# Performance work log

Hardware: AMD Instinct MI355X
Metric: run time of the kernel (lower is better)

Reference implementation:

```python
import jax, jax.numpy as jnp
import numpy as np

B, TGT, SRC, SRC_DIM, TGT_DIM = 4, 4096, 4096, 256, 256
NEG_BIG = 1.0e11   # additive mask constant from the torch code
CLAMP_MIN = -1.0e10


def setup_inputs() -> dict:
    key = jax.random.key(0)
    k1, k2, k3, k4 = jax.random.split(key, 4)
    h_t = jax.random.normal(k1, (B, TGT, TGT_DIM), dtype=jnp.float32)
    h_s = jax.random.normal(k2, (B, SRC, SRC_DIM), dtype=jnp.float32)
    m_s = jax.random.randint(k3, (B, SRC), 0, 2, dtype=jnp.int32)
    # linear_in: nn.Linear(src_dim, tgt_dim, bias=False) -> weight [tgt_dim, src_dim]
    lim = float(np.sqrt(1.0 / SRC_DIM))
    W_in = jax.random.uniform(k4, (TGT_DIM, SRC_DIM), dtype=jnp.float32, minval=-lim, maxval=lim)
    return {"h_t": h_t, "h_s": h_s, "m_s": m_s, "W_in": W_in}


def reference(h_t, h_s, m_s, W_in):
    # 'general' score: h_t @ (linear_in(h_s))^T
    energy = jnp.einsum("bsd,td->bst", h_s, W_in)          # (B, S, tgt_dim)
    scores = jnp.einsum("btd,bsd->bts", h_t, energy)        # (B, T, S)
    m = m_s.astype(scores.dtype)[:, None, :]                 # (B, 1, S)
    scores = scores * m - NEG_BIG * (1.0 - m)
    scores = jax.nn.softmax(jnp.maximum(scores, CLAMP_MIN), axis=-1)
    context = jnp.einsum("bts,bsd->btd", scores, h_s)        # (B, T, src_dim)
    return context, scores
```

## Files before the change

### kernel.cpp

```cpp
#include <hip/hip_runtime.h>
#include <cstdint>
#include <cstddef>

typedef _Float16 f16;
typedef _Float16 half8 __attribute__((ext_vector_type(8)));
typedef float floatx4 __attribute__((ext_vector_type(4)));
typedef unsigned short ushort8 __attribute__((ext_vector_type(8)));

__device__ __forceinline__ void gload_lds16(const void* g, void* l) {
    __builtin_amdgcn_global_load_lds(
        (const __attribute__((address_space(1))) void*)g,
        (__attribute__((address_space(3))) void*)l,
        16, 0, 0);
}

__device__ __forceinline__ unsigned short f32_to_bf16(float f) {
    unsigned u = __float_as_uint(f);
    return (unsigned short)((u + 0x7FFFu + ((u >> 16) & 1u)) >> 16);
}
__device__ __forceinline__ float bf16_to_f32(unsigned short h) {
    return __uint_as_float(((unsigned)h) << 16);
}

__global__ void k_cvt(const float* __restrict__ src, f16* __restrict__ dst, int n8) {
    int i = blockIdx.x * blockDim.x + threadIdx.x;
    if (i >= n8) return;
    const float4* s = (const float4*)src + 2 * (size_t)i;
    float4 a = s[0], b = s[1];
    half8 h;
    h[0] = (f16)a.x; h[1] = (f16)a.y; h[2] = (f16)a.z; h[3] = (f16)a.w;
    h[4] = (f16)b.x; h[5] = (f16)b.y; h[6] = (f16)b.z; h[7] = (f16)b.w;
    ((half8*)dst)[i] = h;
}

__global__ void k_hs(const float* __restrict__ hs, f16* __restrict__ hs16, f16* __restrict__ hsT) {
    int id = blockIdx.x;
    int dt = id & 3;
    int st = (id >> 2) & 63;
    int b  = id >> 8;
    __shared__ f16 tile[64][65];
    int t = threadIdx.x;
    int s0 = st * 64, d0 = dt * 64;
#pragma unroll
    for (int i = 0; i < 16; i++) {
        int e = t + i * 256;
        int r = e >> 6, c = e & 63;
        float v = hs[((size_t)(b * 4096 + s0 + r)) * 256 + d0 + c];
        f16 hv = (f16)v;
        hs16[((size_t)(b * 4096 + s0 + r)) * 256 + d0 + c] = hv;
        tile[r][c] = hv;
    }
    __syncthreads();
#pragma unroll
    for (int i = 0; i < 16; i++) {
        int e = t + i * 256;
        int r = e >> 6, c = e & 63;
        hsT[((size_t)(b * 256 + d0 + r)) * 4096 + s0 + c] = tile[c][r];
    }
}

__global__ __launch_bounds__(256, 2) void k_energy(
    const f16* __restrict__ A,
    const f16* __restrict__ Bt,
    f16* __restrict__ C)
{
    int id = blockIdx.x;
    int tn = id & 1, tm = (id >> 1) & 31, b = id >> 6;
    const f16* Ab = A + (size_t)b * 4096 * 256;

    __shared__ __align__(16) f16 As[128 * 64];
    __shared__ __align__(16) f16 Bs[128 * 64];

    int tid = threadIdx.x;
    int wave = tid >> 6, lane = tid & 63;
    int wr = wave >> 1, wc = wave & 1;
    int lm = lane & 15, lq = lane >> 4;

    floatx4 acc[4][4] = {};
    int r0 = tm * 128, c0 = tn * 128;

    for (int k0 = 0; k0 < 256; k0 += 64) {
#pragma unroll
        for (int i = 0; i < 4; i++) {
            int rbase = wave * 32 + i * 8;
            int row = rbase + (lane >> 3);
            gload_lds16(Ab + (size_t)(r0 + row) * 256 + k0 + (lane & 7) * 8, &As[rbase * 64]);
            gload_lds16(Bt + (size_t)(c0 + row) * 256 + k0 + (lane & 7) * 8, &Bs[rbase * 64]);
        }
        __syncthreads();
        half8 af[4][2], bf[4][2];
#pragma unroll
        for (int mi = 0; mi < 4; mi++)
#pragma unroll
            for (int kk = 0; kk < 2; kk++) {
                af[mi][kk] = *(const half8*)&As[(wr * 64 + mi * 16 + lm) * 64 + kk * 32 + lq * 8];
                bf[mi][kk] = *(const half8*)&Bs[(wc * 64 + mi * 16 + lm) * 64 + kk * 32 + lq * 8];
            }
#pragma unroll
        for (int kk = 0; kk < 2; kk++)
#pragma unroll
            for (int mi = 0; mi < 4; mi++)
#pragma unroll
                for (int ni = 0; ni < 4; ni++)
                    acc[mi][ni] = __builtin_amdgcn_mfma_f32_16x16x32_f16(af[mi][kk], bf[ni][kk], acc[mi][ni], 0, 0, 0);
        __syncthreads();
    }
#pragma unroll
    for (int mi = 0; mi < 4; mi++)
#pragma unroll
        for (int ni = 0; ni < 4; ni++)
#pragma unroll
            for (int r = 0; r < 4; r++) {
                int row = r0 + wr * 64 + mi * 16 + lq * 4 + r;
                int col = c0 + wc * 64 + ni * 16 + lm;
                C[(size_t)(b * 4096 + row) * 256 + col] = (f16)acc[mi][ni][r];
            }
}

__global__ __launch_bounds__(256, 2) void k_scores(
    const f16* __restrict__ A,
    const f16* __restrict__ Bt,
    const int* __restrict__ ms,
    unsigned short* __restrict__ E,
    float* __restrict__ rsum)
{
    int id = blockIdx.x;
    int tn = id & 31, tm = (id >> 5) & 31, b = id >> 10;
    const f16* Ab = A + (size_t)b * 4096 * 256;
    const f16* Bb = Bt + (size_t)b * 4096 * 256;

    __shared__ __align__(16) f16 As[128 * 64];
    __shared__ __align__(16) f16 Bs[128 * 64];

    int tid = threadIdx.x;
    int wave = tid >> 6, lane = tid & 63;
    int wr = wave >> 1, wc = wave & 1;
    int lm = lane & 15, lq = lane >> 4;

    floatx4 acc[4][4] = {};
    int r0 = tm * 128, c0 = tn * 128;

    for (int k0 = 0; k0 < 256; k0 += 64) {
#pragma unroll
        for (int i = 0; i < 4; i++) {
            int rbase = wave * 32 + i * 8;
            int row = rbase + (lane >> 3);
            gload_lds16(Ab + (size_t)(r0 + row) * 256 + k0 + (lane & 7) * 8, &As[rbase * 64]);
            gload_lds16(Bb + (size_t)(c0 + row) * 256 + k0 + (lane & 7) * 8, &Bs[rbase * 64]);
        }
        __syncthreads();
        half8 af[4][2], bf[4][2];
#pragma unroll
        for (int mi = 0; mi < 4; mi++)
#pragma unroll
            for (int kk = 0; kk < 2; kk++) {
                af[mi][kk] = *(const half8*)&As[(wr * 64 + mi * 16 + lm) * 64 + kk * 32 + lq * 8];
                bf[mi][kk] = *(const half8*)&Bs[(wc * 64 + mi * 16 + lm) * 64 + kk * 32 + lq * 8];
            }
#pragma unroll
        for (int kk = 0; kk < 2; kk++)
#pragma unroll
            for (int mi = 0; mi < 4; mi++)
#pragma unroll
                for (int ni = 0; ni < 4; ni++)
                    acc[mi][ni] = __builtin_amdgcn_mfma_f32_16x16x32_f16(af[mi][kk], bf[ni][kk], acc[mi][ni], 0, 0, 0);
        __syncthreads();
    }
    float rs[4][4] = {};
#pragma unroll
    for (int ni = 0; ni < 4; ni++) {
        int col = c0 + wc * 64 + ni * 16 + lm;
        int m = ms[b * 4096 + col];
#pragma unroll
        for (int mi = 0; mi < 4; mi++)
#pragma unroll
            for (int r = 0; r < 4; r++) {
                int row = r0 + wr * 64 + mi * 16 + lq * 4 + r;
                float e = m ? __expf(acc[mi][ni][r]) : 0.0f;
                E[(size_t)(b * 4096 + row) * 4096 + col] = f32_to_bf16(e);
                rs[mi][r] += e;
            }
    }
#pragma unroll
    for (int mi = 0; mi < 4; mi++)
#pragma unroll
        for (int r = 0; r < 4; r++) {
            float v = rs[mi][r];
#pragma unroll
            for (int off = 1; off < 16; off <<= 1)
                v += __shfl_xor(v, off, 16);
            if (lm == 0) {
                int row = r0 + wr * 64 + mi * 16 + lq * 4 + r;
                atomicAdd(&rsum[b * 4096 + row], v);
            }
        }
}

__global__ __launch_bounds__(256, 2) void k_ctx(
    const f16* __restrict__ BtT,
    const unsigned short* __restrict__ E,
    float* __restrict__ P,
    const float* __restrict__ rsum,
    f16* __restrict__ part)
{
    int id = blockIdx.x;
    int ks = id & 3, tt = (id >> 2) & 31, b = id >> 7;
    int tid = threadIdx.x;
    int wave = tid >> 6, lane = tid & 63;
    int lm = lane & 15, lq = lane >> 4;

    __shared__ __align__(16) f16 Bs[8 * 2048];

    int t0 = tt * 128;
    const f16* Bb = BtT + (size_t)b * 256 * 4096;

    float rinv[2];
    size_t rowbase[2];
#pragma unroll
    for (int mi = 0; mi < 2; mi++) {
        int row = t0 + wave * 32 + mi * 16 + lm;
        int gr = b * 4096 + row;
        rinv[mi] = 1.0f / rsum[gr];
        rowbase[mi] = (size_t)gr * 4096;
    }

    int g0 = wave * 2, g1 = wave * 2 + 1;
    int c0g = 2 * (g0 & 3), c1g = 2 * (g1 & 3);
    const f16* gp0 = Bb + (size_t)(lane ^ c0g) * 4096 + g0 * 8;
    const f16* gp1 = Bb + (size_t)(lane ^ c1g) * 4096 + g1 * 8;
    f16* lb0 = &Bs[g0 * 2048];
    f16* lb1 = &Bs[g1 * 2048];

    int rbk[2];
    rbk[0] = (0 * 4 + lq) * 2048 + (lm ^ (2 * lq)) * 8;
    rbk[1] = (1 * 4 + lq) * 2048 + (lm ^ (2 * lq)) * 8;

    floatx4 acc[2][16] = {};
    int sbeg = ks * 1024;

    for (int it = 0; it < 16; it++) {
        int s0 = sbeg + it * 64;
        ushort8 ev[2][2];
#pragma unroll
        for (int mi = 0; mi < 2; mi++)
#pragma unroll
            for (int kk = 0; kk < 2; kk++)
                ev[mi][kk] = *(const ushort8*)(E + rowbase[mi] + s0 + kk * 32 + lq * 8);
#pragma unroll
        for (int R = 0; R < 256; R += 64) {
            gload_lds16(gp0 + (size_t)R * 4096 + s0, lb0 + R * 8);
            gload_lds16(gp1 + (size_t)R * 4096 + s0, lb1 + R * 8);
        }
        half8 af[2][2];
#pragma unroll
        for (int mi = 0; mi < 2; mi++)
#pragma unroll
            for (int kk = 0; kk < 2; kk++) {
                half8 h;
#pragma unroll
                for (int j = 0; j < 8; j++) {
                    float f = bf16_to_f32(ev[mi][kk][j]) * rinv[mi];
                    h[j] = (f16)f;
                }
                af[mi][kk] = h;
            }
        __syncthreads();
#pragma unroll
        for (int mi = 0; mi < 2; mi++)
#pragma unroll
            for (int kk = 0; kk < 2; kk++) {
                float* p = P + rowbase[mi] + s0 + kk * 32 + lq * 8;
                half8 h = af[mi][kk];
                ((float4*)p)[0] = make_float4((float)h[0], (float)h[1], (float)h[2], (float)h[3]);
                ((float4*)p)[1] = make_float4((float)h[4], (float)h[5], (float)h[6], (float)h[7]);
            }
#pragma unroll
        for (int kk = 0; kk < 2; kk++)
#pragma unroll
            for (int ni = 0; ni < 16; ni++) {
                half8 bf = *(const half8*)&Bs[rbk[kk] + ni * 128];
#pragma unroll
                for (int mi = 0; mi < 2; mi++)
                    acc[mi][ni] = __builtin_amdgcn_mfma_f32_16x16x32_f16(af[mi][kk], bf, acc[mi][ni], 0, 0, 0);
            }
        __syncthreads();
    }

    f16* Pp = part + (size_t)ks * 4194304 + (size_t)b * 1048576;
#pragma unroll
    for (int mi = 0; mi < 2; mi++)
#pragma unroll
        for (int ni = 0; ni < 16; ni++)
#pragma unroll
            for (int r = 0; r < 4; r++) {
                int row = t0 + wave * 32 + mi * 16 + lq * 4 + r;
                int col = ni * 16 + lm;
                Pp[(size_t)row * 256 + col] = (f16)acc[mi][ni][r];
            }
}

__global__ void k_red(const f16* __restrict__ part, float* __restrict__ out) {
    size_t i = (size_t)blockIdx.x * 256 + threadIdx.x;
    const half8* p = (const half8*)part;
    half8 a = p[i];
    half8 b = p[i + 524288];
    half8 c = p[i + 1048576];
    half8 d = p[i + 1572864];
    float4 o0, o1;
    o0.x = (float)a[0] + (float)b[0] + (float)c[0] + (float)d[0];
    o0.y = (float)a[1] + (float)b[1] + (float)c[1] + (float)d[1];
    o0.z = (float)a[2] + (float)b[2] + (float)c[2] + (float)d[2];
    o0.w = (float)a[3] + (float)b[3] + (float)c[3] + (float)d[3];
    o1.x = (float)a[4] + (float)b[4] + (float)c[4] + (float)d[4];
    o1.y = (float)a[5] + (float)b[5] + (float)c[5] + (float)d[5];
    o1.z = (float)a[6] + (float)b[6] + (float)c[6] + (float)d[6];
    o1.w = (float)a[7] + (float)b[7] + (float)c[7] + (float)d[7];
    ((float4*)out)[2 * i] = o0;
    ((float4*)out)[2 * i + 1] = o1;
}

extern "C" void kernel_launch(void* const* d_in, const int* in_sizes, int n_in,
                              void* d_out, int out_size, void* d_ws, size_t ws_size,
                              hipStream_t stream) {
    const float* h_t = (const float*)d_in[0];
    const float* h_s = (const float*)d_in[1];
    const int*   m_s = (const int*)d_in[2];
    const float* W   = (const float*)d_in[3];

    float* out = (float*)d_out;
    char* ws = (char*)d_ws;
    f16* h_t16 = (f16*)(ws);
    f16* h_s16 = (f16*)(ws + 8388608);
    f16* h_sT  = (f16*)(ws + 16777216);
    f16* en16  = (f16*)(ws + 25165824);
    f16* W16   = (f16*)(ws + 33554432);
    float* rsum = (float*)(ws + 33685504);
    unsigned short* e16 = (unsigned short*)(ws + 33751040);
    f16* part = (f16*)(ws + 167968768);

    float* ctx = out;
    float* sc  = out + 4194304;

    hipMemsetAsync(rsum, 0, 16384 * sizeof(float), stream);
    k_cvt<<<2048, 256, 0, stream>>>(h_t, h_t16, 524288);
    k_cvt<<<32, 256, 0, stream>>>(W, W16, 8192);
    k_hs<<<1024, 256, 0, stream>>>(h_s, h_s16, h_sT);
    k_energy<<<256, 256, 0, stream>>>(h_s16, W16, en16);
    k_scores<<<4096, 256, 0, stream>>>(h_t16, en16, m_s, e16, rsum);
    k_ctx<<<512, 256, 0, stream>>>(h_sT, e16, sc, rsum, part);
    k_red<<<2048, 256, 0, stream>>>(part, ctx);
}
```

Baseline: 501.2 us.

## Double-buffer LDS tiles in energy, scores and context GEMM kernels

Adds a second LDS buffer to the energy and scores GEMMs and unrolls the four K-steps so the next tile's global-to-LDS load is issued before computing on the current tile. This roughly halves the barriers per step. The context kernel gets a ping-pong LDS buffer and register prefetch of the next E chunk, overlapping memory latency with the MFMA work. LDS use doubles (64KB per block in the GEMMs) and register pressure rises, which may lower occupancy under the launch bound of 2 blocks.

```diff
diff --git a/kernel.cpp b/kernel.cpp
--- a/kernel.cpp
+++ b/kernel.cpp
@@ -59,6 +59,33 @@
     }
 }
 
+#define GE_STAGE(AS, BS, K0) do { \
+    _Pragma("unroll") \
+    for (int i_ = 0; i_ < 4; i_++) { \
+        int rbase_ = wave * 32 + i_ * 8; \
+        int row_ = rbase_ + (lane >> 3); \
+        gload_lds16(Ab + (size_t)(r0 + row_) * 256 + (K0) + (lane & 7) * 8, &AS[rbase_ * 64]); \
+        gload_lds16(Bsrc + (size_t)(c0 + row_) * 256 + (K0) + (lane & 7) * 8, &BS[rbase_ * 64]); \
+    } } while (0)
+
+#define GE_COMPUTE(AS, BS) do { \
+    half8 af_[4][2], bf_[4][2]; \
+    _Pragma("unroll") \
+    for (int mi_ = 0; mi_ < 4; mi_++) \
+        _Pragma("unroll") \
+        for (int kk_ = 0; kk_ < 2; kk_++) { \
+            af_[mi_][kk_] = *(const half8*)&AS[(wr * 64 + mi_ * 16 + lm) * 64 + kk_ * 32 + lq * 8]; \
+            bf_[mi_][kk_] = *(const half8*)&BS[(wc * 64 + mi_ * 16 + lm) * 64 + kk_ * 32 + lq * 8]; \
+        } \
+    _Pragma("unroll") \
+    for (int kk_ = 0; kk_ < 2; kk_++) \
+        _Pragma("unroll") \
+        for (int mi_ = 0; mi_ < 4; mi_++) \
+            _Pragma("unroll") \
+            for (int ni_ = 0; ni_ < 4; ni_++) \
+                acc[mi_][ni_] = __builtin_amdgcn_mfma_f32_16x16x32_f16(af_[mi_][kk_], bf_[ni_][kk_], acc[mi_][ni_], 0, 0, 0); \
+    } while (0)
+
 __global__ __launch_bounds__(256, 2) void k_energy(
     const f16* __restrict__ A,
     const f16* __restrict__ Bt,
@@ -67,9 +94,12 @@
     int id = blockIdx.x;
     int tn = id & 1, tm = (id >> 1) & 31, b = id >> 6;
     const f16* Ab = A + (size_t)b * 4096 * 256;
-
-    __shared__ __align__(16) f16 As[128 * 64];
-    __shared__ __align__(16) f16 Bs[128 * 64];
+    const f16* Bsrc = Bt;
+
+    __shared__ __align__(16) f16 As0[128 * 64];
+    __shared__ __align__(16) f16 Bs0[128 * 64];
+    __shared__ __align__(16) f16 As1[128 * 64];
+    __shared__ __align__(16) f16 Bs1[128 * 64];
 
     int tid = threadIdx.x;
     int wave = tid >> 6, lane = tid & 63;
@@ -79,32 +109,19 @@
     floatx4 acc[4][4] = {};
     int r0 = tm * 128, c0 = tn * 128;
 
-    for (int k0 = 0; k0 < 256; k0 += 64) {
-#pragma unroll
-        for (int i = 0; i < 4; i++) {
-            int rbase = wave * 32 + i * 8;
-            int row = rbase + (lane >> 3);
-            gload_lds16(Ab + (size_t)(r0 + row) * 256 + k0 + (lane & 7) * 8, &As[rbase * 64]);
-            gload_lds16(Bt + (size_t)(c0 + row) * 256 + k0 + (lane & 7) * 8, &Bs[rbase * 64]);
-        }
-        __syncthreads();
-        half8 af[4][2], bf[4][2];
-#pragma unroll
-        for (int mi = 0; mi < 4; mi++)
-#pragma unroll
-            for (int kk = 0; kk < 2; kk++) {
-                af[mi][kk] = *(const half8*)&As[(wr * 64 + mi * 16 + lm) * 64 + kk * 32 + lq * 8];
-                bf[mi][kk] = *(const half8*)&Bs[(wc * 64 + mi * 16 + lm) * 64 + kk * 32 + lq * 8];
-            }
-#pragma unroll
-        for (int kk = 0; kk < 2; kk++)
-#pragma unroll
-            for (int mi = 0; mi < 4; mi++)
-#pragma unroll
-                for (int ni = 0; ni < 4; ni++)
-                    acc[mi][ni] = __builtin_amdgcn_mfma_f32_16x16x32_f16(af[mi][kk], bf[ni][kk], acc[mi][ni], 0, 0, 0);
-        __syncthreads();
-    }
+    GE_STAGE(As0, Bs0, 0);
+    __syncthreads();
+    GE_STAGE(As1, Bs1, 64);
+    GE_COMPUTE(As0, Bs0);
+    __syncthreads();
+    GE_STAGE(As0, Bs0, 128);
+    GE_COMPUTE(As1, Bs1);
+    __syncthreads();
+    GE_STAGE(As1, Bs1, 192);
+    GE_COMPUTE(As0, Bs0);
+    __syncthreads();
+    GE_COMPUTE(As1, Bs1);
+
 #pragma unroll
     for (int mi = 0; mi < 4; mi++)
 #pragma unroll
@@ -127,10 +144,12 @@
     int id = blockIdx.x;
     int tn = id & 31, tm = (id >> 5) & 31, b = id >> 10;
     const f16* Ab = A + (size_t)b * 4096 * 256;
-    const f16* Bb = Bt + (size_t)b * 4096 * 256;
-
-    __shared__ __align__(16) f16 As[128 * 64];
-    __shared__ __align__(16) f16 Bs[128 * 64];
+    const f16* Bsrc = Bt + (size_t)b * 4096 * 256;
+
+    __shared__ __align__(16) f16 As0[128 * 64];
+    __shared__ __align__(16) f16 Bs0[128 * 64];
+    __shared__ __align__(16) f16 As1[128 * 64];
+    __shared__ __align__(16) f16 Bs1[128 * 64];
 
     int tid = threadIdx.x;
     int wave = tid >> 6, lane = tid & 63;
@@ -140,32 +159,19 @@
     floatx4 acc[4][4] = {};
     int r0 = tm * 128, c0 = tn * 128;
 
-    for (int k0 = 0; k0 < 256; k0 += 64) {
-#pragma unroll
-        for (int i = 0; i < 4; i++) {
-            int rbase = wave * 32 + i * 8;
-            int row = rbase + (lane >> 3);
-            gload_lds16(Ab + (size_t)(r0 + row) * 256 + k0 + (lane & 7) * 8, &As[rbase * 64]);
-            gload_lds16(Bb + (size_t)(c0 + row) * 256 + k0 + (lane & 7) * 8, &Bs[rbase * 64]);
-        }
-        __syncthreads();
-        half8 af[4][2], bf[4][2];
-#pragma unroll
-        for (int mi = 0; mi < 4; mi++)
-#pragma unroll
-            for (int kk = 0; kk < 2; kk++) {
-                af[mi][kk] = *(const half8*)&As[(wr * 64 + mi * 16 + lm) * 64 + kk * 32 + lq * 8];
-                bf[mi][kk] = *(const half8*)&Bs[(wc * 64 + mi * 16 + lm) * 64 + kk * 32 + lq * 8];
-            }
-#pragma unroll
-        for (int kk = 0; kk < 2; kk++)
-#pragma unroll
-            for (int mi = 0; mi < 4; mi++)
-#pragma unroll
-                for (int ni = 0; ni < 4; ni++)
-                    acc[mi][ni] = __builtin_amdgcn_mfma_f32_16x16x32_f16(af[mi][kk], bf[ni][kk], acc[mi][ni], 0, 0, 0);
-        __syncthreads();
-    }
+    GE_STAGE(As0, Bs0, 0);
+    __syncthreads();
+    GE_STAGE(As1, Bs1, 64);
+    GE_COMPUTE(As0, Bs0);
+    __syncthreads();
+    GE_STAGE(As0, Bs0, 128);
+    GE_COMPUTE(As1, Bs1);
+    __syncthreads();
+    GE_STAGE(As1, Bs1, 192);
+    GE_COMPUTE(As0, Bs0);
+    __syncthreads();
+    GE_COMPUTE(As1, Bs1);
+
     float rs[4][4] = {};
 #pragma unroll
     for (int ni = 0; ni < 4; ni++) {
@@ -209,7 +215,8 @@
     int wave = tid >> 6, lane = tid & 63;
     int lm = lane & 15, lq = lane >> 4;
 
-    __shared__ __align__(16) f16 Bs[8 * 2048];
+    __shared__ __align__(16) f16 Bs0[8 * 2048];
+    __shared__ __align__(16) f16 Bs1[8 * 2048];
 
     int t0 = tt * 128;
     const f16* Bb = BtT + (size_t)b * 256 * 4096;
@@ -228,8 +235,7 @@
     int c0g = 2 * (g0 & 3), c1g = 2 * (g1 & 3);
     const f16* gp0 = Bb + (size_t)(lane ^ c0g) * 4096 + g0 * 8;
     const f16* gp1 = Bb + (size_t)(lane ^ c1g) * 4096 + g1 * 8;
-    f16* lb0 = &Bs[g0 * 2048];
-    f16* lb1 = &Bs[g1 * 2048];
+    int lds_off0 = g0 * 2048, lds_off1 = g1 * 2048;
 
     int rbk[2];
     rbk[0] = (0 * 4 + lq) * 2048 + (lm ^ (2 * lq)) * 8;
@@ -238,53 +244,78 @@
     floatx4 acc[2][16] = {};
     int sbeg = ks * 1024;
 
-    for (int it = 0; it < 16; it++) {
-        int s0 = sbeg + it * 64;
-        ushort8 ev[2][2];
-#pragma unroll
-        for (int mi = 0; mi < 2; mi++)
-#pragma unroll
-            for (int kk = 0; kk < 2; kk++)
-                ev[mi][kk] = *(const ushort8*)(E + rowbase[mi] + s0 + kk * 32 + lq * 8);
-#pragma unroll
-        for (int R = 0; R < 256; R += 64) {
-            gload_lds16(gp0 + (size_t)R * 4096 + s0, lb0 + R * 8);
-            gload_lds16(gp1 + (size_t)R * 4096 + s0, lb1 + R * 8);
-        }
-        half8 af[2][2];
-#pragma unroll
-        for (int mi = 0; mi < 2; mi++)
-#pragma unroll
-            for (int kk = 0; kk < 2; kk++) {
-                half8 h;
-#pragma unroll
-                for (int j = 0; j < 8; j++) {
-                    float f = bf16_to_f32(ev[mi][kk][j]) * rinv[mi];
-                    h[j] = (f16)f;
-                }
-                af[mi][kk] = h;
-            }
-        __syncthreads();
-#pragma unroll
-        for (int mi = 0; mi < 2; mi++)
-#pragma unroll
-            for (int kk = 0; kk < 2; kk++) {
-                float* p = P + rowbase[mi] + s0 + kk * 32 + lq * 8;
-                half8 h = af[mi][kk];
-                ((float4*)p)[0] = make_float4((float)h[0], (float)h[1], (float)h[2], (float)h[3]);
-                ((float4*)p)[1] = make_float4((float)h[4], (float)h[5], (float)h[6], (float)h[7]);
-            }
+    ushort8 ev[2][2];
+#pragma unroll
+    for (int mi = 0; mi < 2; mi++)
 #pragma unroll
         for (int kk = 0; kk < 2; kk++)
-#pragma unroll
-            for (int ni = 0; ni < 16; ni++) {
-                half8 bf = *(const half8*)&Bs[rbk[kk] + ni * 128];
-#pragma unroll
-                for (int mi = 0; mi < 2; mi++)
-                    acc[mi][ni] = __builtin_amdgcn_mfma_f32_16x16x32_f16(af[mi][kk], bf, acc[mi][ni], 0, 0, 0);
-            }
-        __syncthreads();
-    }
+            ev[mi][kk] = *(const ushort8*)(E + rowbase[mi] + sbeg + kk * 32 + lq * 8);
+#pragma unroll
+    for (int R = 0; R < 256; R += 64) {
+        gload_lds16(gp0 + (size_t)R * 4096 + sbeg, &Bs0[lds_off0 + R * 8]);
+        gload_lds16(gp1 + (size_t)R * 4096 + sbeg, &Bs0[lds_off1 + R * 8]);
+    }
+    __syncthreads();
+
+#define CTX_ITER(IT, BSR, BSW) do { \
+    ushort8 evn_[2][2]; \
+    if ((IT) < 15) { \
+        int s0n_ = sbeg + ((IT) + 1) * 64; \
+        _Pragma("unroll") \
+        for (int mi = 0; mi < 2; mi++) \
+            _Pragma("unroll") \
+            for (int kk = 0; kk < 2; kk++) \
+                evn_[mi][kk] = *(const ushort8*)(E + rowbase[mi] + s0n_ + kk * 32 + lq * 8); \
+        _Pragma("unroll") \
+        for (int R = 0; R < 256; R += 64) { \
+            gload_lds16(gp0 + (size_t)R * 4096 + s0n_, &BSW[lds_off0 + R * 8]); \
+            gload_lds16(gp1 + (size_t)R * 4096 + s0n_, &BSW[lds_off1 + R * 8]); \
+        } \
+    } \
+    int s0c_ = sbeg + (IT) * 64; \
+    half8 af_[2][2]; \
+    _Pragma("unroll") \
+    for (int mi = 0; mi < 2; mi++) \
+        _Pragma("unroll") \
+        for (int kk = 0; kk < 2; kk++) { \
+            half8 h_; \
+            _Pragma("unroll") \
+            for (int j = 0; j < 8; j++) \
+                h_[j] = (f16)(bf16_to_f32(ev[mi][kk][j]) * rinv[mi]); \
+            af_[mi][kk] = h_; \
+        } \
+    _Pragma("unroll") \
+    for (int mi = 0; mi < 2; mi++) \
+        _Pragma("unroll") \
+        for (int kk = 0; kk < 2; kk++) { \
+            float* p_ = P + rowbase[mi] + s0c_ + kk * 32 + lq * 8; \
+            half8 h_ = af_[mi][kk]; \
+            ((float4*)p_)[0] = make_float4((float)h_[0], (float)h_[1], (float)h_[2], (float)h_[3]); \
+            ((float4*)p_)[1] = make_float4((float)h_[4], (float)h_[5], (float)h_[6], (float)h_[7]); \
+        } \
+    _Pragma("unroll") \
+    for (int kk = 0; kk < 2; kk++) \
+        _Pragma("unroll") \
+        for (int ni = 0; ni < 16; ni++) { \
+            half8 bf_ = *(const half8*)&BSR[rbk[kk] + ni * 128]; \
+            _Pragma("unroll") \
+            for (int mi = 0; mi < 2; mi++) \
+                acc[mi][ni] = __builtin_amdgcn_mfma_f32_16x16x32_f16(af_[mi][kk], bf_, acc[mi][ni], 0, 0, 0); \
+        } \
+    __syncthreads(); \
+    if ((IT) < 15) { \
+        _Pragma("unroll") \
+        for (int mi = 0; mi < 2; mi++) \
+            _Pragma("unroll") \
+            for (int kk = 0; kk < 2; kk++) \
+                ev[mi][kk] = evn_[mi][kk]; \
+    } } while (0)
+
+    for (int it = 0; it < 16; it += 2) {
+        CTX_ITER(it, Bs0, Bs1);
+        CTX_ITER(it + 1, Bs1, Bs0);
+    }
+#undef CTX_ITER
 
     f16* Pp = part + (size_t)ks * 4194304 + (size_t)b * 1048576;
 #pragma unroll
```

Result: slower. 537.4 us (+7.2%).

## Double-buffer LDS tiles in context kernel and merge conversion launches

Applied to the files above, without the earlier changes.

The context GEMM kernel now uses two LDS buffers. It prefetches the next s-tile of transposed h_s while the MFMAs run on the current one, which removes one __syncthreads per iteration and hides global-to-LDS latency. The two fp32-to-fp16 conversion launches are merged into a single kernel to save one launch. The cost is twice the LDS per block (64KB), which may limit the requested occupancy of 2 blocks per CU.

```diff
diff --git a/kernel.cpp b/kernel.cpp
--- a/kernel.cpp
+++ b/kernel.cpp
@@ -22,15 +22,20 @@
     return __uint_as_float(((unsigned)h) << 16);
 }
 
-__global__ void k_cvt(const float* __restrict__ src, f16* __restrict__ dst, int n8) {
+__global__ void k_cvt2(const float* __restrict__ srcA, f16* __restrict__ dstA, int n8a,
+                       const float* __restrict__ srcB, f16* __restrict__ dstB, int n8b) {
     int i = blockIdx.x * blockDim.x + threadIdx.x;
-    if (i >= n8) return;
-    const float4* s = (const float4*)src + 2 * (size_t)i;
+    const float* src;
+    f16* dst;
+    int j;
+    if (i < n8a) { src = srcA; dst = dstA; j = i; }
+    else { j = i - n8a; if (j >= n8b) return; src = srcB; dst = dstB; }
+    const float4* s = (const float4*)src + 2 * (size_t)j;
     float4 a = s[0], b = s[1];
     half8 h;
     h[0] = (f16)a.x; h[1] = (f16)a.y; h[2] = (f16)a.z; h[3] = (f16)a.w;
     h[4] = (f16)b.x; h[5] = (f16)b.y; h[6] = (f16)b.z; h[7] = (f16)b.w;
-    ((half8*)dst)[i] = h;
+    ((half8*)dst)[j] = h;
 }
 
 __global__ void k_hs(const float* __restrict__ hs, f16* __restrict__ hs16, f16* __restrict__ hsT) {
@@ -209,7 +214,8 @@
     int wave = tid >> 6, lane = tid & 63;
     int lm = lane & 15, lq = lane >> 4;
 
-    __shared__ __align__(16) f16 Bs[8 * 2048];
+    __shared__ __align__(16) f16 Bs0[8 * 2048];
+    __shared__ __align__(16) f16 Bs1[8 * 2048];
 
     int t0 = tt * 128;
     const f16* Bb = BtT + (size_t)b * 256 * 4096;
@@ -228,8 +234,7 @@
     int c0g = 2 * (g0 & 3), c1g = 2 * (g1 & 3);
     const f16* gp0 = Bb + (size_t)(lane ^ c0g) * 4096 + g0 * 8;
     const f16* gp1 = Bb + (size_t)(lane ^ c1g) * 4096 + g1 * 8;
-    f16* lb0 = &Bs[g0 * 2048];
-    f16* lb1 = &Bs[g1 * 2048];
+    int lds_off0 = g0 * 2048, lds_off1 = g1 * 2048;
 
     int rbk[2];
     rbk[0] = (0 * 4 + lq) * 2048 + (lm ^ (2 * lq)) * 8;
@@ -238,53 +243,66 @@
     floatx4 acc[2][16] = {};
     int sbeg = ks * 1024;
 
-    for (int it = 0; it < 16; it++) {
-        int s0 = sbeg + it * 64;
-        ushort8 ev[2][2];
-#pragma unroll
-        for (int mi = 0; mi < 2; mi++)
-#pragma unroll
-            for (int kk = 0; kk < 2; kk++)
-                ev[mi][kk] = *(const ushort8*)(E + rowbase[mi] + s0 + kk * 32 + lq * 8);
-#pragma unroll
-        for (int R = 0; R < 256; R += 64) {
-            gload_lds16(gp0 + (size_t)R * 4096 + s0, lb0 + R * 8);
-            gload_lds16(gp1 + (size_t)R * 4096 + s0, lb1 + R * 8);
-        }
-        half8 af[2][2];
-#pragma unroll
-        for (int mi = 0; mi < 2; mi++)
-#pragma unroll
-            for (int kk = 0; kk < 2; kk++) {
-                half8 h;
-#pragma unroll
-                for (int j = 0; j < 8; j++) {
-                    float f = bf16_to_f32(ev[mi][kk][j]) * rinv[mi];
-                    h[j] = (f16)f;
-                }
-                af[mi][kk] = h;
-            }
-        __syncthreads();
-#pragma unroll
-        for (int mi = 0; mi < 2; mi++)
-#pragma unroll
-            for (int kk = 0; kk < 2; kk++) {
-                float* p = P + rowbase[mi] + s0 + kk * 32 + lq * 8;
-                half8 h = af[mi][kk];
-                ((float4*)p)[0] = make_float4((float)h[0], (float)h[1], (float)h[2], (float)h[3]);
-                ((float4*)p)[1] = make_float4((float)h[4], (float)h[5], (float)h[6], (float)h[7]);
-            }
-#pragma unroll
-        for (int kk = 0; kk < 2; kk++)
-#pragma unroll
-            for (int ni = 0; ni < 16; ni++) {
-                half8 bf = *(const half8*)&Bs[rbk[kk] + ni * 128];
-#pragma unroll
-                for (int mi = 0; mi < 2; mi++)
-                    acc[mi][ni] = __builtin_amdgcn_mfma_f32_16x16x32_f16(af[mi][kk], bf, acc[mi][ni], 0, 0, 0);
-            }
-        __syncthreads();
-    }
+#pragma unroll
+    for (int R = 0; R < 256; R += 64) {
+        gload_lds16(gp0 + (size_t)R * 4096 + sbeg, &Bs0[lds_off0 + R * 8]);
+        gload_lds16(gp1 + (size_t)R * 4096 + sbeg, &Bs0[lds_off1 + R * 8]);
+    }
+    __syncthreads();
+
+#define CTX_ITER(IT, BSR, BSW) do { \
+    int s0c_ = sbeg + (IT) * 64; \
+    ushort8 ev_[2][2]; \
+    _Pragma("unroll") \
+    for (int mi = 0; mi < 2; mi++) \
+        _Pragma("unroll") \
+        for (int kk = 0; kk < 2; kk++) \
+            ev_[mi][kk] = *(const ushort8*)(E + rowbase[mi] + s0c_ + kk * 32 + lq * 8); \
+    if ((IT) < 15) { \
+        int s0n_ = s0c_ + 64; \
+        _Pragma("unroll") \
+        for (int R = 0; R < 256; R += 64) { \
+            gload_lds16(gp0 + (size_t)R * 4096 + s0n_, &BSW[lds_off0 + R * 8]); \
+            gload_lds16(gp1 + (size_t)R * 4096 + s0n_, &BSW[lds_off1 + R * 8]); \
+        } \
+    } \
+    half8 af_[2][2]; \
+    _Pragma("unroll") \
+    for (int mi = 0; mi < 2; mi++) \
+        _Pragma("unroll") \
+        for (int kk = 0; kk < 2; kk++) { \
+            half8 h_; \
+            _Pragma("unroll") \
+            for (int j = 0; j < 8; j++) \
+                h_[j] = (f16)(bf16_to_f32(ev_[mi][kk][j]) * rinv[mi]); \
+            af_[mi][kk] = h_; \
+        } \
+    _Pragma("unroll") \
+    for (int mi = 0; mi < 2; mi++) \
+        _Pragma("unroll") \
+        for (int kk = 0; kk < 2; kk++) { \
+            float* p_ = P + rowbase[mi] + s0c_ + kk * 32 + lq * 8; \
+            half8 h_ = af_[mi][kk]; \
+            ((float4*)p_)[0] = make_float4((float)h_[0], (float)h_[1], (float)h_[2], (float)h_[3]); \
+            ((float4*)p_)[1] = make_float4((float)h_[4], (float)h_[5], (float)h_[6], (float)h_[7]); \
+        } \
+    _Pragma("unroll") \
+    for (int kk = 0; kk < 2; kk++) \
+        _Pragma("unroll") \
+        for (int ni = 0; ni < 16; ni++) { \
+            half8 bf_ = *(const half8*)&BSR[rbk[kk] + ni * 128]; \
+            _Pragma("unroll") \
+            for (int mi = 0; mi < 2; mi++) \
+                acc[mi][ni] = __builtin_amdgcn_mfma_f32_16x16x32_f16(af_[mi][kk], bf_, acc[mi][ni], 0, 0, 0); \
+        } \
+    __syncthreads(); \
+    } while (0)
+
+    for (int it = 0; it < 16; it += 2) {
+        CTX_ITER(it, Bs0, Bs1);
+        CTX_ITER(it + 1, Bs1, Bs0);
+    }
+#undef CTX_ITER
 
     f16* Pp = part + (size_t)ks * 4194304 + (size_t)b * 1048576;
 #pragma unroll
@@ -342,8 +360,7 @@
     float* sc  = out + 4194304;
 
     hipMemsetAsync(rsum, 0, 16384 * sizeof(float), stream);
-    k_cvt<<<2048, 256, 0, stream>>>(h_t, h_t16, 524288);
-    k_cvt<<<32, 256, 0, stream>>>(W, W16, 8192);
+    k_cvt2<<<2080, 256, 0, stream>>>(h_t, h_t16, 524288, W, W16, 8192);
     k_hs<<<1024, 256, 0, stream>>>(h_s, h_s16, h_sT);
     k_energy<<<256, 256, 0, stream>>>(h_s16, W16, en16);
     k_scores<<<4096, 256, 0, stream>>>(h_t16, en16, m_s, e16, rsum);
```

Result: faster. 490.7 us (-2.1%).
